# Kernel optimization log

Measured on AMD Instinct MI355X. Metric: run time of the kernel, lower is better.

Reference implementation:

```python
import jax, jax.numpy as jnp
from jax import lax
import numpy as np

B = 4096

def _conv(x, w, b):
    # x: [B,C,H,W], w: [O,I,3,3] torch OIHW layout, VALID, stride 1
    y = lax.conv_general_dilated(x, w, (1, 1), 'VALID',
                                 dimension_numbers=('NCHW', 'OIHW', 'NCHW'))
    return y + b[None, :, None, None]

def _pool2(x):
    return lax.reduce_window(x, -jnp.inf, lax.max, (1, 1, 2, 2), (1, 1, 2, 2), 'VALID')

def _lin(x, w, b):
    # torch Linear: y = x @ W^T + b, W: [out, in]
    return x @ w.T + b

def setup_inputs() -> dict:
    key = jax.random.key(0)
    ks = jax.random.split(key, 24)
    def w(k, shape, fan_in):
        return (jax.random.normal(k, shape, dtype=jnp.float32) / np.sqrt(fan_in)).astype(jnp.float32)
    inp = {
        'x':      jax.random.normal(ks[0], (B, 1, 28, 28), dtype=jnp.float32),
        'c1_w':   w(ks[1], (50, 1, 3, 3), 9),      'c1_b':  jnp.zeros((50,), jnp.float32),
        'c2_w':   w(ks[2], (50, 50, 3, 3), 450),   'c2_b':  jnp.zeros((50,), jnp.float32),
        'c3_w':   w(ks[3], (50, 50, 3, 3), 450),   'c3_b':  jnp.zeros((50,), jnp.float32),
        'l1c1_w': w(ks[4], (500, 50 * 13 * 13), 50 * 13 * 13), 'l1c1_b': jnp.zeros((500,), jnp.float32),
        'l2c1_w': w(ks[5], (10, 500), 500),        'l2c1_b': jnp.zeros((10,), jnp.float32),
        'l1c2_w': w(ks[6], (500, 50 * 5 * 5), 50 * 5 * 5),     'l1c2_b': jnp.zeros((500,), jnp.float32),
        'l2c2_w': w(ks[7], (10, 500), 500),        'l2c2_b': jnp.zeros((10,), jnp.float32),
        'l1_w':   w(ks[8], (500, 50), 50),         'l1_b':  jnp.zeros((500,), jnp.float32),
        'l2_w':   w(ks[9], (10, 500), 500),        'l2_b':  jnp.zeros((10,), jnp.float32),
        'd1_w':   w(ks[10], (2, 50 * 13 * 13), 50 * 13 * 13),  'd1_b':  jnp.zeros((2,), jnp.float32),
        'd2_w':   w(ks[11], (2, 50 * 5 * 5), 50 * 5 * 5),      'd2_b':  jnp.zeros((2,), jnp.float32),
    }
    return inp

def reference(x, c1_w, c1_b, c2_w, c2_b, c3_w, c3_b,
              l1c1_w, l1c1_b, l2c1_w, l2c1_b,
              l1c2_w, l1c2_b, l2c2_w, l2c2_b,
              l1_w, l1_b, l2_w, l2_b, d1_w, d1_b, d2_w, d2_b):
    b = x.shape[0]
    # stage 1
    h1 = _pool2(jax.nn.relu(_conv(x, c1_w, c1_b)))           # [B,50,13,13]
    f1 = h1.reshape(b, 50 * 13 * 13)
    exit1 = jnp.argmax(_lin(f1, d1_w, d1_b), axis=1) == 0     # [B] bool
    out1 = _lin(_lin(f1, l1c1_w, l1c1_b), l2c1_w, l2c1_b)     # [B,10] (no relu, as in source)
    # stage 2 (computed densely; selection below replicates the gather/scatter routing)
    h2 = _pool2(jax.nn.relu(_conv(h1, c2_w, c2_b)))          # [B,50,5,5]
    f2 = h2.reshape(b, 50 * 5 * 5)
    exit2 = jnp.argmax(_lin(f2, d2_w, d2_b), axis=1) == 0
    out2 = _lin(_lin(f2, l1c2_w, l1c2_b), l2c2_w, l2c2_b)
    # stage 3
    h3 = _pool2(jax.nn.relu(_conv(h2, c3_w, c3_b)))          # [B,50,1,1]
    f3 = h3.reshape(b, 50)
    out3 = _lin(jax.nn.relu(_lin(f3, l1_w, l1_b)), l2_w, l2_b)
    sel = jnp.where(exit1[:, None], out1, jnp.where(exit2[:, None], out2, out3))
    # original returns cat(out1_subset, out2_subset, out3_subset) + an index order;
    # we return the equivalent per-sample outputs in original batch order.
    return jax.nn.log_softmax(sel, axis=1)
```

## Files before the change

kernel.cpp:

```cpp
#include <hip/hip_runtime.h>
#include <hip/hip_bf16.h>
#include <cstdint>


typedef __bf16 bf16_t;
typedef __bf16 bf16x8 __attribute__((ext_vector_type(8)));
typedef float  f32x4  __attribute__((ext_vector_type(4)));

#define B_IMG 4096

__global__ __launch_bounds__(256) void conv1_pool(
    const float* __restrict__ x, const float* __restrict__ w1,
    const float* __restrict__ b1, float* __restrict__ h1, int nimg)
{
    __shared__ float ws[450];
    __shared__ float bs[50];
    const int t = threadIdx.x;
    for (int i = t; i < 450; i += 256) ws[i] = w1[i];
    if (t < 50) bs[t] = b1[t];
    __syncthreads();

    const int idx = blockIdx.x * 256 + t;
    if (idx >= nimg * 169) return;
    const int b   = idx / 169;
    const int pos = idx % 169;
    const int py = pos / 13, px = pos % 13;

    const float* xp = x + (size_t)b * 784 + (2 * py) * 28 + 2 * px;
    float p[4][4];
#pragma unroll
    for (int r = 0; r < 4; ++r)
#pragma unroll
        for (int c = 0; c < 4; ++c) p[r][c] = xp[r * 28 + c];

    float* hb = h1 + (size_t)b * 8480 + pos;
    if (pos < 30) h1[(size_t)b * 8480 + 8450 + pos] = 0.f;

    for (int oc = 0; oc < 50; ++oc) {
        const float* wp = &ws[oc * 9];
        const float w00 = wp[0], w01 = wp[1], w02 = wp[2];
        const float w10 = wp[3], w11 = wp[4], w12 = wp[5];
        const float w20 = wp[6], w21 = wp[7], w22 = wp[8];
        float a[2][2];
#pragma unroll
        for (int dy = 0; dy < 2; ++dy)
#pragma unroll
            for (int dx = 0; dx < 2; ++dx) {
                a[dy][dx] = p[dy + 0][dx + 0] * w00 + p[dy + 0][dx + 1] * w01 + p[dy + 0][dx + 2] * w02
                          + p[dy + 1][dx + 0] * w10 + p[dy + 1][dx + 1] * w11 + p[dy + 1][dx + 2] * w12
                          + p[dy + 2][dx + 0] * w20 + p[dy + 2][dx + 1] * w21 + p[dy + 2][dx + 2] * w22;
            }
        float v = fmaxf(fmaxf(a[0][0], a[0][1]), fmaxf(a[1][0], a[1][1])) + bs[oc];
        hb[oc * 169] = fmaxf(v, 0.f);
    }
}

__global__ __launch_bounds__(256) void w2_transpose(
    const float* __restrict__ w2, float* __restrict__ w2p)
{
    const int idx = blockIdx.x * 256 + threadIdx.x;
    if (idx >= 50 * 600) return;
    const int ic = idx / 600, r = idx % 600, oc = r / 12, j = r % 12;
    w2p[idx] = (j < 9) ? w2[oc * 450 + ic * 9 + j] : 0.f;
}

__global__ __launch_bounds__(256) void conv2_pool(
    const float* __restrict__ h1, const float* __restrict__ w2p,
    const float* __restrict__ b2, float* __restrict__ h2)
{
    __shared__ float in[8450];
    __shared__ __align__(16) float wbuf[2][2400];
    const int b = blockIdx.x;
    const int t = threadIdx.x;
    for (int i = t; i < 8450; i += 256) in[i] = h1[(size_t)b * 8480 + i];
    {
        const float4* src = (const float4*)w2p;
        float4* dst = (float4*)wbuf[0];
        for (int s = t; s < 600; s += 256) dst[s] = src[s];
    }
    __syncthreads();
    if (t < 30) h2[(size_t)b * 1280 + 1250 + t] = 0.f;

    const int ocg = t / 25;
    const int pos = t % 25;
    const int py = pos / 5, px = pos % 5;
    const int oc0 = ocg * 5;
    const bool act = (t < 250);

    float acc[5][4];
#pragma unroll
    for (int j = 0; j < 5; ++j)
#pragma unroll
        for (int q = 0; q < 4; ++q) acc[j][q] = 0.f;

    const float* ib = &in[(2 * py) * 13 + 2 * px];

    for (int ic0 = 0; ic0 < 50; ic0 += 4) {
        const int cur = (ic0 >> 2) & 1;
        if (ic0 + 4 < 50) {
            const int nxt = cur ^ 1;
            const int nic2 = (50 - ic0 - 4 < 4) ? (50 - ic0 - 4) : 4;
            const float4* src = (const float4*)(w2p + (size_t)(ic0 + 4) * 600);
            float4* dst = (float4*)wbuf[nxt];
            for (int s = t; s < nic2 * 150; s += 256) dst[s] = src[s];
        }
        if (act) {
            const int nic = (50 - ic0 < 4) ? (50 - ic0) : 4;
            for (int icl = 0; icl < nic; ++icl) {
                const int ic = ic0 + icl;
                float p[4][4];
                const float* ip = ib + ic * 169;
#pragma unroll
                for (int r = 0; r < 4; ++r)
#pragma unroll
                    for (int c = 0; c < 4; ++c) p[r][c] = ip[r * 13 + c];
                const float* wl = &wbuf[cur][icl * 600 + oc0 * 12];
#pragma unroll
                for (int j = 0; j < 5; ++j) {
                    const f32x4 wv0 = *(const f32x4*)(wl + j * 12);
                    const f32x4 wv1 = *(const f32x4*)(wl + j * 12 + 4);
                    const f32x4 wv2 = *(const f32x4*)(wl + j * 12 + 8);
                    const float w00 = wv0[0], w01 = wv0[1], w02 = wv0[2];
                    const float w10 = wv0[3], w11 = wv1[0], w12 = wv1[1];
                    const float w20 = wv1[2], w21 = wv1[3], w22 = wv2[0];
#pragma unroll
                    for (int dy = 0; dy < 2; ++dy)
#pragma unroll
                        for (int dx = 0; dx < 2; ++dx) {
                            acc[j][dy * 2 + dx] +=
                                  p[dy + 0][dx + 0] * w00 + p[dy + 0][dx + 1] * w01 + p[dy + 0][dx + 2] * w02
                                + p[dy + 1][dx + 0] * w10 + p[dy + 1][dx + 1] * w11 + p[dy + 1][dx + 2] * w12
                                + p[dy + 2][dx + 0] * w20 + p[dy + 2][dx + 1] * w21 + p[dy + 2][dx + 2] * w22;
                        }
                }
            }
        }
        __syncthreads();
    }

    if (act) {
#pragma unroll
        for (int j = 0; j < 5; ++j) {
            float v = fmaxf(fmaxf(acc[j][0], acc[j][1]), fmaxf(acc[j][2], acc[j][3]));
            h2[(size_t)b * 1280 + (oc0 + j) * 25 + pos] = fmaxf(v + b2[oc0 + j], 0.f);
        }
    }
}

__global__ __launch_bounds__(256) void conv3_pool(
    const float* __restrict__ h2, const float* __restrict__ w3,
    const float* __restrict__ b3, float* __restrict__ f3)
{
    __shared__ float in[5000];
    const int blk = blockIdx.x;
    const int t = threadIdx.x;
    for (int i = t; i < 5000; i += 256) {
        const int img = i / 1250, off = i % 1250;
        in[i] = h2[(size_t)(blk * 4 + img) * 1280 + off];
    }
    __syncthreads();
    const int il = t >> 6;
    const int oc = t & 63;
    if (oc >= 50) return;

    const float* ip0 = &in[il * 1250];
    float a00 = 0.f, a01 = 0.f, a10 = 0.f, a11 = 0.f;
    for (int ic = 0; ic < 50; ++ic) {
        float p[4][4];
        const float* ip = ip0 + ic * 25;
#pragma unroll
        for (int r = 0; r < 4; ++r)
#pragma unroll
            for (int c = 0; c < 4; ++c) p[r][c] = ip[r * 5 + c];
        const float* wp = &w3[((size_t)oc * 50 + ic) * 9];
        const float w00 = wp[0], w01 = wp[1], w02 = wp[2];
        const float w10 = wp[3], w11 = wp[4], w12 = wp[5];
        const float w20 = wp[6], w21 = wp[7], w22 = wp[8];
        a00 += p[0][0]*w00 + p[0][1]*w01 + p[0][2]*w02 + p[1][0]*w10 + p[1][1]*w11 + p[1][2]*w12 + p[2][0]*w20 + p[2][1]*w21 + p[2][2]*w22;
        a01 += p[0][1]*w00 + p[0][2]*w01 + p[0][3]*w02 + p[1][1]*w10 + p[1][2]*w11 + p[1][3]*w12 + p[2][1]*w20 + p[2][2]*w21 + p[2][3]*w22;
        a10 += p[1][0]*w00 + p[1][1]*w01 + p[1][2]*w02 + p[2][0]*w10 + p[2][1]*w11 + p[2][2]*w12 + p[3][0]*w20 + p[3][1]*w21 + p[3][2]*w22;
        a11 += p[1][1]*w00 + p[1][2]*w01 + p[1][3]*w02 + p[2][1]*w10 + p[2][2]*w11 + p[2][3]*w12 + p[3][1]*w20 + p[3][2]*w21 + p[3][3]*w22;
    }
    float v = fmaxf(fmaxf(a00, a01), fmaxf(a10, a11)) + b3[oc];
    f3[(size_t)(blk * 4 + il) * 50 + oc] = fmaxf(v, 0.f);
}

__global__ __launch_bounds__(256) void exit_kernel(
    const float* __restrict__ F, int ldf, int K,
    const float* __restrict__ dw, const float* __restrict__ db, int* __restrict__ e)
{
    const int b = blockIdx.x;
    const int t = threadIdx.x;
    const float* f = F + (size_t)b * ldf;
    float s0 = 0.f, s1 = 0.f;
    for (int i = t; i < K; i += 256) {
        const float v = f[i];
        s0 += v * dw[i];
        s1 += v * dw[K + i];
    }
    __shared__ float r0[256];
    __shared__ float r1[256];
    r0[t] = s0; r1[t] = s1;
    __syncthreads();
    for (int s = 128; s > 0; s >>= 1) {
        if (t < s) { r0[t] += r0[t + s]; r1[t] += r1[t + s]; }
        __syncthreads();
    }
    if (t == 0) e[b] = (r0[0] + db[0] >= r1[0] + db[1]) ? 1 : 0;
}

__global__ __launch_bounds__(256) void w_to_bf16(
    const float* __restrict__ src, bf16_t* __restrict__ dst, int N, int K, int Kp, int total)
{
    const int idx = blockIdx.x * 256 + threadIdx.x;
    if (idx >= total) return;
    const int n = idx / Kp, k = idx % Kp;
    const float v = (n < N && k < K) ? src[(size_t)n * K + k] : 0.f;
    dst[idx] = (bf16_t)v;
}

__global__ __launch_bounds__(256) void gemm_f32a_bf16w(
    const float* __restrict__ A, int lda,
    const bf16_t* __restrict__ W,
    const float* __restrict__ bias, float* __restrict__ C0, float* __restrict__ C1,
    int Kp, int khalf, int Nout, int ldc)
{
    __shared__ __align__(16) bf16_t As[128 * 40];
    __shared__ __align__(16) bf16_t Bs[64 * 40];

    const int t = threadIdx.x;
    const int m0 = blockIdx.x * 128;
    const int n0 = blockIdx.y * 64;
    const int kz = blockIdx.z;
    const int kbeg = kz ? khalf : 0;
    const int kend = kz ? Kp : khalf;
    float* C = kz ? C1 : C0;

    const int wave = t >> 6;
    const int lane = t & 63;
    const int wm = (wave >> 1) * 64;
    const int wn = (wave & 1) * 32;
    const int quad = lane >> 4;
    const int lr = lane & 15;

    f32x4 acc[4][2];
#pragma unroll
    for (int i = 0; i < 4; ++i)
#pragma unroll
        for (int j = 0; j < 2; ++j) acc[i][j] = (f32x4)0.f;

    const int ar = t >> 2;
    const int ac = (t & 3) * 8;

    for (int k0 = kbeg; k0 < kend; k0 += 32) {
        __syncthreads();
#pragma unroll
        for (int h = 0; h < 2; ++h) {
            const float* ap = A + (size_t)(m0 + ar + h * 64) * lda + k0 + ac;
            const float4 f0 = *(const float4*)ap;
            const float4 f1 = *(const float4*)(ap + 4);
            bf16x8 v;
            v[0] = (bf16_t)f0.x; v[1] = (bf16_t)f0.y; v[2] = (bf16_t)f0.z; v[3] = (bf16_t)f0.w;
            v[4] = (bf16_t)f1.x; v[5] = (bf16_t)f1.y; v[6] = (bf16_t)f1.z; v[7] = (bf16_t)f1.w;
            *(bf16x8*)&As[(ar + h * 64) * 40 + ac] = v;
        }
        *(uint4*)&Bs[ar * 40 + ac] = *(const uint4*)&W[(size_t)(n0 + ar) * Kp + k0 + ac];
        __syncthreads();

        bf16x8 af[4], bfr[2];
#pragma unroll
        for (int i = 0; i < 4; ++i)
            af[i] = *(const bf16x8*)&As[(wm + i * 16 + lr) * 40 + quad * 8];
#pragma unroll
        for (int j = 0; j < 2; ++j)
            bfr[j] = *(const bf16x8*)&Bs[(wn + j * 16 + lr) * 40 + quad * 8];
#pragma unroll
        for (int i = 0; i < 4; ++i)
#pragma unroll
            for (int j = 0; j < 2; ++j)
                acc[i][j] = __builtin_amdgcn_mfma_f32_16x16x32_bf16(af[i], bfr[j], acc[i][j], 0, 0, 0);
    }

#pragma unroll
    for (int j = 0; j < 2; ++j) {
        const int n = n0 + wn + j * 16 + lr;
        const float bv = (kz == 0 && n < Nout) ? bias[n] : 0.f;
#pragma unroll
        for (int i = 0; i < 4; ++i) {
            const int mrow = m0 + wm + i * 16 + quad * 4;
#pragma unroll
            for (int r = 0; r < 4; ++r)
                C[(size_t)(mrow + r) * ldc + n] = acc[i][j][r] + bv;
        }
    }
}

__global__ __launch_bounds__(256) void lin10(
    const float* __restrict__ U, const float* __restrict__ U2, int ldu,
    const float* __restrict__ W, const float* __restrict__ bias,
    float* __restrict__ out)
{
    __shared__ float red[16][10][17];
    const int t = threadIdx.x;
    const int ks = t & 15;
    const int il = t >> 4;
    const int b  = blockIdx.x * 16 + il;
    const float* u = U + (size_t)b * ldu;

    float acc[10];
#pragma unroll
    for (int o = 0; o < 10; ++o) acc[o] = 0.f;

    if (U2) {
        const float* u2 = U2 + (size_t)b * ldu;
        for (int i = 0; i < 31; ++i) {
            const int k = ks + i * 16;
            const float uv = u[k] + u2[k];
#pragma unroll
            for (int o = 0; o < 10; ++o) acc[o] += uv * W[o * 500 + k];
        }
        const int k = ks + 496;
        if (k < 500) {
            const float uv = u[k] + u2[k];
#pragma unroll
            for (int o = 0; o < 10; ++o) acc[o] += uv * W[o * 500 + k];
        }
    } else {
        for (int i = 0; i < 31; ++i) {
            const int k = ks + i * 16;
            const float uv = u[k];
#pragma unroll
            for (int o = 0; o < 10; ++o) acc[o] += uv * W[o * 500 + k];
        }
        const int k = ks + 496;
        if (k < 500) {
            const float uv = u[k];
#pragma unroll
            for (int o = 0; o < 10; ++o) acc[o] += uv * W[o * 500 + k];
        }
    }
#pragma unroll
    for (int o = 0; o < 10; ++o) red[il][o][ks] = acc[o];
    __syncthreads();
    if (t < 160) {
        const int il2 = t / 10, o = t - il2 * 10;
        float s = 0.f;
#pragma unroll
        for (int q = 0; q < 16; ++q) s += red[il2][o][q];
        out[(size_t)(blockIdx.x * 16 + il2) * 10 + o] = s + bias[o];
    }
}

__global__ __launch_bounds__(256) void lin500(
    const float* __restrict__ f3, const float* __restrict__ w,
    const float* __restrict__ bias, float* __restrict__ u3)
{
    __shared__ float fs[50];
    const int b = blockIdx.x;
    const int t = threadIdx.x;
    if (t < 50) fs[t] = f3[(size_t)b * 50 + t];
    __syncthreads();
    for (int o = t; o < 500; o += 256) {
        float s = 0.f;
#pragma unroll
        for (int k = 0; k < 50; ++k) s += fs[k] * w[o * 50 + k];
        u3[(size_t)b * 512 + o] = fmaxf(s + bias[o], 0.f);
    }
}

__global__ __launch_bounds__(256) void final_select(
    const int* __restrict__ e1, const int* __restrict__ e2,
    const float* __restrict__ o1, const float* __restrict__ o2,
    const float* __restrict__ o3, float* __restrict__ out)
{
    const int b = blockIdx.x * 256 + threadIdx.x;
    if (b >= B_IMG) return;
    const float* src = e1[b] ? o1 : (e2[b] ? o2 : o3);
    src += (size_t)b * 10;
    float v[10];
    float m = -3.4e38f;
#pragma unroll
    for (int o = 0; o < 10; ++o) { v[o] = src[o]; m = fmaxf(m, v[o]); }
    float s = 0.f;
#pragma unroll
    for (int o = 0; o < 10; ++o) s += expf(v[o] - m);
    const float ls = logf(s);
#pragma unroll
    for (int o = 0; o < 10; ++o) out[(size_t)b * 10 + o] = v[o] - m - ls;
}

static inline size_t align256(size_t v) { return (v + 255) & ~(size_t)255; }

extern "C" void kernel_launch(void* const* d_in, const int* in_sizes, int n_in,
                              void* d_out, int out_size, void* d_ws, size_t ws_size,
                              hipStream_t stream)
{
    const float* x     = (const float*)d_in[0];
    const float* c1w   = (const float*)d_in[1];
    const float* c1b   = (const float*)d_in[2];
    const float* c2w   = (const float*)d_in[3];
    const float* c2b   = (const float*)d_in[4];
    const float* c3w   = (const float*)d_in[5];
    const float* c3b   = (const float*)d_in[6];
    const float* l1c1w = (const float*)d_in[7];
    const float* l1c1b = (const float*)d_in[8];
    const float* l2c1w = (const float*)d_in[9];
    const float* l2c1b = (const float*)d_in[10];
    const float* l1c2w = (const float*)d_in[11];
    const float* l1c2b = (const float*)d_in[12];
    const float* l2c2w = (const float*)d_in[13];
    const float* l2c2b = (const float*)d_in[14];
    const float* l1w   = (const float*)d_in[15];
    const float* l1b   = (const float*)d_in[16];
    const float* l2w   = (const float*)d_in[17];
    const float* l2b   = (const float*)d_in[18];
    const float* d1w   = (const float*)d_in[19];
    const float* d1b   = (const float*)d_in[20];
    const float* d2w   = (const float*)d_in[21];
    const float* d2b   = (const float*)d_in[22];

    size_t off = 0;
    const size_t oWb1  = off; off = align256(off + (size_t)512 * 8480 * 2);
    const size_t oWb2  = off; off = align256(off + (size_t)512 * 1280 * 2);
    const size_t oW2P  = off; off = align256(off + (size_t)50 * 600 * 4);
    const size_t oOut1 = off; off = align256(off + (size_t)B_IMG * 10 * 4);
    const size_t oOut2 = off; off = align256(off + (size_t)B_IMG * 10 * 4);
    const size_t oOut3 = off; off = align256(off + (size_t)B_IMG * 10 * 4);
    const size_t oE1   = off; off = align256(off + (size_t)B_IMG * 4);
    const size_t oE2   = off; off = align256(off + (size_t)B_IMG * 4);
    const size_t persist = off;

    auto chunk_bytes = [](int C) {
        size_t s = 0;
        s += align256((size_t)C * 8480 * 4);
        s += align256((size_t)C * 1280 * 4);
        s += align256((size_t)C * 512 * 4);
        s += align256((size_t)C * 512 * 4);
        s += align256((size_t)C * 50 * 4);
        return s;
    };
    int C = B_IMG;
    while (C > 256 && persist + chunk_bytes(C) > ws_size) C >>= 1;

    char* ws = (char*)d_ws;
    bf16_t* Wb1  = (bf16_t*)(ws + oWb1);
    bf16_t* Wb2  = (bf16_t*)(ws + oWb2);
    float*  w2p  = (float*) (ws + oW2P);
    float*  out1 = (float*) (ws + oOut1);
    float*  out2 = (float*) (ws + oOut2);
    float*  out3 = (float*) (ws + oOut3);
    int*    e1   = (int*)   (ws + oE1);
    int*    e2   = (int*)   (ws + oE2);

    size_t co = persist;
    float* h1 = (float*)(ws + co); co += align256((size_t)C * 8480 * 4);
    float* h2 = (float*)(ws + co); co += align256((size_t)C * 1280 * 4);
    float* u  = (float*)(ws + co); co += align256((size_t)C * 512 * 4);
    float* up = (float*)(ws + co); co += align256((size_t)C * 512 * 4);
    float* f3 = (float*)(ws + co); co += align256((size_t)C * 50 * 4);

    float* out = (float*)d_out;

    w_to_bf16<<<(512 * 8480) / 256, 256, 0, stream>>>(l1c1w, Wb1, 500, 8450, 8480, 512 * 8480);
    w_to_bf16<<<(512 * 1280) / 256, 256, 0, stream>>>(l1c2w, Wb2, 500, 1250, 1280, 512 * 1280);
    w2_transpose<<<(50 * 600 + 255) / 256, 256, 0, stream>>>(c2w, w2p);

    for (int b0 = 0; b0 < B_IMG; b0 += C) {
        conv1_pool<<<(C * 169 + 255) / 256, 256, 0, stream>>>(x + (size_t)b0 * 784, c1w, c1b, h1, C);
        exit_kernel<<<C, 256, 0, stream>>>(h1, 8480, 8450, d1w, d1b, e1 + b0);
        gemm_f32a_bf16w<<<dim3(C / 128, 8, 2), 256, 0, stream>>>(h1, 8480, Wb1, l1c1b, u, up, 8480, 4256, 500, 512);
        lin10<<<C / 16, 256, 0, stream>>>(u, up, 512, l2c1w, l2c1b, out1 + (size_t)b0 * 10);

        conv2_pool<<<C, 256, 0, stream>>>(h1, w2p, c2b, h2);
        exit_kernel<<<C, 256, 0, stream>>>(h2, 1280, 1250, d2w, d2b, e2 + b0);
        gemm_f32a_bf16w<<<dim3(C / 128, 8, 2), 256, 0, stream>>>(h2, 1280, Wb2, l1c2b, u, up, 1280, 640, 500, 512);
        lin10<<<C / 16, 256, 0, stream>>>(u, up, 512, l2c2w, l2c2b, out2 + (size_t)b0 * 10);

        conv3_pool<<<C / 4, 256, 0, stream>>>(h2, c3w, c3b, f3);
        lin500<<<C, 256, 0, stream>>>(f3, l1w, l1b, u);
        lin10<<<C / 16, 256, 0, stream>>>(u, nullptr, 512, l2w, l2b, out3 + (size_t)b0 * 10);
    }

    final_select<<<B_IMG / 256, 256, 0, stream>>>(e1, e2, out1, out2, out3, out);

    (void)in_sizes; (void)n_in; (void)out_size; (void)ws_size;
}
```

Baseline: 776.0 us.

## Merge independent stages into role-dispatched fused kernels and drop batch chunking

Turns each former kernel into a device role function and groups independent work (conv1 with the weight conversions, GEMM1 with conv2 and exit1, GEMM2 with conv3, lin10 and exit2, and so on) into a few kernels that pick a role from the block index. The whole batch is now processed at once with full-size buffers instead of a chunk loop. This is meant to cut launch count and serialization and let concurrent stages fill the GPU. In exchange, shared memory becomes dynamic and sized to the largest role, which may lower occupancy for the light roles. The layout also assumes the workspace is big enough and reuses h1 as scratch after it is consumed.

```diff
diff --git a/kernel.cpp b/kernel.cpp
--- a/kernel.cpp
+++ b/kernel.cpp
@@ -9,19 +9,20 @@
 
 #define B_IMG 4096
 
-__global__ __launch_bounds__(256) void conv1_pool(
+
+__device__ void role_conv1(char* smem, int blk,
     const float* __restrict__ x, const float* __restrict__ w1,
-    const float* __restrict__ b1, float* __restrict__ h1, int nimg)
-{
-    __shared__ float ws[450];
-    __shared__ float bs[50];
+    const float* __restrict__ b1, float* __restrict__ h1)
+{
+    float* ws = (float*)smem;
+    float* bs = ws + 456;
     const int t = threadIdx.x;
     for (int i = t; i < 450; i += 256) ws[i] = w1[i];
     if (t < 50) bs[t] = b1[t];
     __syncthreads();
 
-    const int idx = blockIdx.x * 256 + t;
-    if (idx >= nimg * 169) return;
+    const int idx = blk * 256 + t;
+    if (idx >= B_IMG * 169) return;
     const int b   = idx / 169;
     const int pos = idx % 169;
     const int py = pos / 13, px = pos % 13;
@@ -55,27 +56,35 @@
     }
 }
 
-__global__ __launch_bounds__(256) void w2_transpose(
-    const float* __restrict__ w2, float* __restrict__ w2p)
-{
-    const int idx = blockIdx.x * 256 + threadIdx.x;
+__device__ void role_wb16(int blk, const float* __restrict__ src,
+                          bf16_t* __restrict__ dst, int N, int K, int Kp, int total)
+{
+    const int idx = blk * 256 + threadIdx.x;
+    if (idx >= total) return;
+    const int n = idx / Kp, k = idx % Kp;
+    const float v = (n < N && k < K) ? src[(size_t)n * K + k] : 0.f;
+    dst[idx] = (bf16_t)v;
+}
+
+__device__ void role_w2t(int blk, const float* __restrict__ w2, float* __restrict__ w2p)
+{
+    const int idx = blk * 256 + threadIdx.x;
     if (idx >= 50 * 600) return;
     const int ic = idx / 600, r = idx % 600, oc = r / 12, j = r % 12;
     w2p[idx] = (j < 9) ? w2[oc * 450 + ic * 9 + j] : 0.f;
 }
 
-__global__ __launch_bounds__(256) void conv2_pool(
+__device__ void role_conv2(char* smem, int b,
     const float* __restrict__ h1, const float* __restrict__ w2p,
     const float* __restrict__ b2, float* __restrict__ h2)
 {
-    __shared__ float in[8450];
-    __shared__ __align__(16) float wbuf[2][2400];
-    const int b = blockIdx.x;
+    float* in   = (float*)smem;
+    float* wbuf = in + 8452;
     const int t = threadIdx.x;
     for (int i = t; i < 8450; i += 256) in[i] = h1[(size_t)b * 8480 + i];
     {
         const float4* src = (const float4*)w2p;
-        float4* dst = (float4*)wbuf[0];
+        float4* dst = (float4*)wbuf;
         for (int s = t; s < 600; s += 256) dst[s] = src[s];
     }
     __syncthreads();
@@ -101,7 +110,7 @@
             const int nxt = cur ^ 1;
             const int nic2 = (50 - ic0 - 4 < 4) ? (50 - ic0 - 4) : 4;
             const float4* src = (const float4*)(w2p + (size_t)(ic0 + 4) * 600);
-            float4* dst = (float4*)wbuf[nxt];
+            float4* dst = (float4*)(wbuf + nxt * 2400);
             for (int s = t; s < nic2 * 150; s += 256) dst[s] = src[s];
         }
         if (act) {
@@ -114,7 +123,7 @@
                 for (int r = 0; r < 4; ++r)
 #pragma unroll
                     for (int c = 0; c < 4; ++c) p[r][c] = ip[r * 13 + c];
-                const float* wl = &wbuf[cur][icl * 600 + oc0 * 12];
+                const float* wl = wbuf + cur * 2400 + icl * 600 + oc0 * 12;
 #pragma unroll
                 for (int j = 0; j < 5; ++j) {
                     const f32x4 wv0 = *(const f32x4*)(wl + j * 12);
@@ -147,12 +156,11 @@
     }
 }
 
-__global__ __launch_bounds__(256) void conv3_pool(
+__device__ void role_conv3(char* smem, int blk,
     const float* __restrict__ h2, const float* __restrict__ w3,
     const float* __restrict__ b3, float* __restrict__ f3)
 {
-    __shared__ float in[5000];
-    const int blk = blockIdx.x;
+    float* in = (float*)smem;
     const int t = threadIdx.x;
     for (int i = t; i < 5000; i += 256) {
         const int img = i / 1250, off = i % 1250;
@@ -185,11 +193,12 @@
     f3[(size_t)(blk * 4 + il) * 50 + oc] = fmaxf(v, 0.f);
 }
 
-__global__ __launch_bounds__(256) void exit_kernel(
+__device__ void role_exit(char* smem, int b,
     const float* __restrict__ F, int ldf, int K,
     const float* __restrict__ dw, const float* __restrict__ db, int* __restrict__ e)
 {
-    const int b = blockIdx.x;
+    float* r0 = (float*)smem;
+    float* r1 = r0 + 256;
     const int t = threadIdx.x;
     const float* f = F + (size_t)b * ldf;
     float s0 = 0.f, s1 = 0.f;
@@ -198,8 +207,6 @@
         s0 += v * dw[i];
         s1 += v * dw[K + i];
     }
-    __shared__ float r0[256];
-    __shared__ float r1[256];
     r0[t] = s0; r1[t] = s1;
     __syncthreads();
     for (int s = 128; s > 0; s >>= 1) {
@@ -209,29 +216,18 @@
     if (t == 0) e[b] = (r0[0] + db[0] >= r1[0] + db[1]) ? 1 : 0;
 }
 
-__global__ __launch_bounds__(256) void w_to_bf16(
-    const float* __restrict__ src, bf16_t* __restrict__ dst, int N, int K, int Kp, int total)
-{
-    const int idx = blockIdx.x * 256 + threadIdx.x;
-    if (idx >= total) return;
-    const int n = idx / Kp, k = idx % Kp;
-    const float v = (n < N && k < K) ? src[(size_t)n * K + k] : 0.f;
-    dst[idx] = (bf16_t)v;
-}
-
-__global__ __launch_bounds__(256) void gemm_f32a_bf16w(
-    const float* __restrict__ A, int lda,
-    const bf16_t* __restrict__ W,
+__device__ void role_gemm(char* smem, int g,
+    const float* __restrict__ A, int lda, const bf16_t* __restrict__ W,
     const float* __restrict__ bias, float* __restrict__ C0, float* __restrict__ C1,
     int Kp, int khalf, int Nout, int ldc)
 {
-    __shared__ __align__(16) bf16_t As[128 * 40];
-    __shared__ __align__(16) bf16_t Bs[64 * 40];
-
-    const int t = threadIdx.x;
-    const int m0 = blockIdx.x * 128;
-    const int n0 = blockIdx.y * 64;
-    const int kz = blockIdx.z;
+    bf16_t* As = (bf16_t*)smem;
+    bf16_t* Bs = As + 128 * 40;
+
+    const int t = threadIdx.x;
+    const int m0 = (g & 31) * 128;
+    const int n0 = ((g >> 5) & 7) * 64;
+    const int kz = g >> 8;
     const int kbeg = kz ? khalf : 0;
     const int kend = kz ? Kp : khalf;
     float* C = kz ? C1 : C0;
@@ -295,16 +291,16 @@
     }
 }
 
-__global__ __launch_bounds__(256) void lin10(
+__device__ void role_lin10(char* smem, int blk,
     const float* __restrict__ U, const float* __restrict__ U2, int ldu,
     const float* __restrict__ W, const float* __restrict__ bias,
     float* __restrict__ out)
 {
-    __shared__ float red[16][10][17];
+    float* red = (float*)smem;
     const int t = threadIdx.x;
     const int ks = t & 15;
     const int il = t >> 4;
-    const int b  = blockIdx.x * 16 + il;
+    const int b  = blk * 16 + il;
     const float* u = U + (size_t)b * ldu;
 
     float acc[10];
@@ -340,23 +336,22 @@
         }
     }
 #pragma unroll
-    for (int o = 0; o < 10; ++o) red[il][o][ks] = acc[o];
+    for (int o = 0; o < 10; ++o) red[(il * 10 + o) * 17 + ks] = acc[o];
     __syncthreads();
     if (t < 160) {
         const int il2 = t / 10, o = t - il2 * 10;
         float s = 0.f;
 #pragma unroll
-        for (int q = 0; q < 16; ++q) s += red[il2][o][q];
-        out[(size_t)(blockIdx.x * 16 + il2) * 10 + o] = s + bias[o];
-    }
-}
-
-__global__ __launch_bounds__(256) void lin500(
+        for (int q = 0; q < 16; ++q) s += red[(il2 * 10 + o) * 17 + q];
+        out[(size_t)(blk * 16 + il2) * 10 + o] = s + bias[o];
+    }
+}
+
+__device__ void role_lin500(char* smem, int b,
     const float* __restrict__ f3, const float* __restrict__ w,
     const float* __restrict__ bias, float* __restrict__ u3)
 {
-    __shared__ float fs[50];
-    const int b = blockIdx.x;
+    float* fs = (float*)smem;
     const int t = threadIdx.x;
     if (t < 50) fs[t] = f3[(size_t)b * 50 + t];
     __syncthreads();
@@ -366,6 +361,63 @@
         for (int k = 0; k < 50; ++k) s += fs[k] * w[o * 50 + k];
         u3[(size_t)b * 512 + o] = fmaxf(s + bias[o], 0.f);
     }
+}
+
+
+__global__ __launch_bounds__(256) void k_prep(
+    const float* x, const float* c1w, const float* c1b, float* h1,
+    const float* l1c1w, bf16_t* Wb1, const float* l1c2w, bf16_t* Wb2,
+    const float* c2w, float* w2p)
+{
+    extern __shared__ char smem[];
+    const int g = blockIdx.x;
+    if (g < 2704)        role_conv1(smem, g, x, c1w, c1b, h1);
+    else if (g < 19664)  role_wb16(g - 2704, l1c1w, Wb1, 500, 8450, 8480, 512 * 8480);
+    else if (g < 22224)  role_wb16(g - 19664, l1c2w, Wb2, 500, 1250, 1280, 512 * 1280);
+    else                 role_w2t(g - 22224, c2w, w2p);
+}
+
+__global__ __launch_bounds__(256) void k_stage1(
+    const float* h1, const bf16_t* Wb1, const float* l1c1b, float* u, float* up,
+    const float* d1w, const float* d1b, int* e1,
+    const float* w2p, const float* c2b, float* h2)
+{
+    extern __shared__ char smem[];
+    const int g = blockIdx.x;
+    if (g < 512)         role_gemm(smem, g, h1, 8480, Wb1, l1c1b, u, up, 8480, 4256, 500, 512);
+    else if (g < 4608)   role_conv2(smem, g - 512, h1, w2p, c2b, h2);
+    else                 role_exit(smem, g - 4608, h1, 8480, 8450, d1w, d1b, e1);
+}
+
+__global__ __launch_bounds__(256) void k_stage2(
+    const float* h2, const bf16_t* Wb2, const float* l1c2b, float* v, float* vp,
+    const float* d2w, const float* d2b, int* e2,
+    const float* c3w, const float* c3b, float* f3,
+    const float* u, const float* up, const float* l2c1w, const float* l2c1b, float* out1)
+{
+    extern __shared__ char smem[];
+    const int g = blockIdx.x;
+    if (g < 512)         role_gemm(smem, g, h2, 1280, Wb2, l1c2b, v, vp, 1280, 640, 500, 512);
+    else if (g < 1536)   role_conv3(smem, g - 512, h2, c3w, c3b, f3);
+    else if (g < 1792)   role_lin10(smem, g - 1536, u, up, 512, l2c1w, l2c1b, out1);
+    else                 role_exit(smem, g - 1792, h2, 1280, 1250, d2w, d2b, e2);
+}
+
+__global__ __launch_bounds__(256) void k_stage3a(
+    const float* v, const float* vp, const float* l2c2w, const float* l2c2b, float* out2,
+    const float* f3, const float* l1w, const float* l1b, float* u3)
+{
+    extern __shared__ char smem[];
+    const int g = blockIdx.x;
+    if (g < 256)         role_lin10(smem, g, v, vp, 512, l2c2w, l2c2b, out2);
+    else                 role_lin500(smem, g - 256, f3, l1w, l1b, u3);
+}
+
+__global__ __launch_bounds__(256) void k_stage3b(
+    const float* u3, const float* l2w, const float* l2b, float* out3)
+{
+    extern __shared__ char smem[];
+    role_lin10(smem, blockIdx.x, u3, nullptr, 512, l2w, l2b, out3);
 }
 
 __global__ __launch_bounds__(256) void final_select(
@@ -428,19 +480,11 @@
     const size_t oOut3 = off; off = align256(off + (size_t)B_IMG * 10 * 4);
     const size_t oE1   = off; off = align256(off + (size_t)B_IMG * 4);
     const size_t oE2   = off; off = align256(off + (size_t)B_IMG * 4);
-    const size_t persist = off;
-
-    auto chunk_bytes = [](int C) {
-        size_t s = 0;
-        s += align256((size_t)C * 8480 * 4);
-        s += align256((size_t)C * 1280 * 4);
-        s += align256((size_t)C * 512 * 4);
-        s += align256((size_t)C * 512 * 4);
-        s += align256((size_t)C * 50 * 4);
-        return s;
-    };
-    int C = B_IMG;
-    while (C > 256 && persist + chunk_bytes(C) > ws_size) C >>= 1;
+    const size_t oH1   = off; off = align256(off + (size_t)B_IMG * 8480 * 4);
+    const size_t oH2   = off; off = align256(off + (size_t)B_IMG * 1280 * 4);
+    const size_t oU    = off; off = align256(off + (size_t)B_IMG * 512 * 4);
+    const size_t oUP   = off; off = align256(off + (size_t)B_IMG * 512 * 4);
+    const size_t oF3   = off; off = align256(off + (size_t)B_IMG * 50 * 4);
 
     char* ws = (char*)d_ws;
     bf16_t* Wb1  = (bf16_t*)(ws + oWb1);
@@ -451,36 +495,23 @@
     float*  out3 = (float*) (ws + oOut3);
     int*    e1   = (int*)   (ws + oE1);
     int*    e2   = (int*)   (ws + oE2);
-
-    size_t co = persist;
-    float* h1 = (float*)(ws + co); co += align256((size_t)C * 8480 * 4);
-    float* h2 = (float*)(ws + co); co += align256((size_t)C * 1280 * 4);
-    float* u  = (float*)(ws + co); co += align256((size_t)C * 512 * 4);
-    float* up = (float*)(ws + co); co += align256((size_t)C * 512 * 4);
-    float* f3 = (float*)(ws + co); co += align256((size_t)C * 50 * 4);
+    float*  h1   = (float*) (ws + oH1);
+    float*  h2   = (float*) (ws + oH2);
+    float*  u    = (float*) (ws + oU);
+    float*  up   = (float*) (ws + oUP);
+    float*  f3   = (float*) (ws + oF3);
+    float*  v    = h1;
+    float*  vp   = h1 + (size_t)B_IMG * 512;
+    float*  u3   = h1 + (size_t)B_IMG * 1024;
 
     float* out = (float*)d_out;
 
-    w_to_bf16<<<(512 * 8480) / 256, 256, 0, stream>>>(l1c1w, Wb1, 500, 8450, 8480, 512 * 8480);
-    w_to_bf16<<<(512 * 1280) / 256, 256, 0, stream>>>(l1c2w, Wb2, 500, 1250, 1280, 512 * 1280);
-    w2_transpose<<<(50 * 600 + 255) / 256, 256, 0, stream>>>(c2w, w2p);
-
-    for (int b0 = 0; b0 < B_IMG; b0 += C) {
-        conv1_pool<<<(C * 169 + 255) / 256, 256, 0, stream>>>(x + (size_t)b0 * 784, c1w, c1b, h1, C);
-        exit_kernel<<<C, 256, 0, stream>>>(h1, 8480, 8450, d1w, d1b, e1 + b0);
-        gemm_f32a_bf16w<<<dim3(C / 128, 8, 2), 256, 0, stream>>>(h1, 8480, Wb1, l1c1b, u, up, 8480, 4256, 500, 512);
-        lin10<<<C / 16, 256, 0, stream>>>(u, up, 512, l2c1w, l2c1b, out1 + (size_t)b0 * 10);
-
-        conv2_pool<<<C, 256, 0, stream>>>(h1, w2p, c2b, h2);
-        exit_kernel<<<C, 256, 0, stream>>>(h2, 1280, 1250, d2w, d2b, e2 + b0);
-        gemm_f32a_bf16w<<<dim3(C / 128, 8, 2), 256, 0, stream>>>(h2, 1280, Wb2, l1c2b, u, up, 1280, 640, 500, 512);
-        lin10<<<C / 16, 256, 0, stream>>>(u, up, 512, l2c2w, l2c2b, out2 + (size_t)b0 * 10);
-
-        conv3_pool<<<C / 4, 256, 0, stream>>>(h2, c3w, c3b, f3);
-        lin500<<<C, 256, 0, stream>>>(f3, l1w, l1b, u);
-        lin10<<<C / 16, 256, 0, stream>>>(u, nullptr, 512, l2w, l2b, out3 + (size_t)b0 * 10);
-    }
-
+    k_prep<<<22342, 256, 2048, stream>>>(x, c1w, c1b, h1, l1c1w, Wb1, l1c2w, Wb2, c2w, w2p);
+    k_stage1<<<8704, 256, 53248, stream>>>(h1, Wb1, l1c1b, u, up, d1w, d1b, e1, w2p, c2b, h2);
+    k_stage2<<<5888, 256, 20000, stream>>>(h2, Wb2, l1c2b, v, vp, d2w, d2b, e2,
+                                           c3w, c3b, f3, u, up, l2c1w, l2c1b, out1);
+    k_stage3a<<<4352, 256, 10880, stream>>>(v, vp, l2c2w, l2c2b, out2, f3, l1w, l1b, u3);
+    k_stage3b<<<256, 256, 10880, stream>>>(u3, l2w, l2b, out3);
     final_select<<<B_IMG / 256, 256, 0, stream>>>(e1, e2, out1, out2, out3, out);
 
     (void)in_sizes; (void)n_in; (void)out_size; (void)ws_size;
```

Measured after the change: 740.8 us. 4.5% less time.
